# Kernel optimization log

Measured on AMD Instinct MI355X. Metric: run time of the kernel, lower is better.

The kernel has to match this reference:

```python
import jax, jax.numpy as jnp
import numpy as np

N = 8192; E = 131072; K = 20; IN_DIM = 3; HID = 256; N_CLASSES = 32


def setup_inputs():
    key = jax.random.key(0)
    ks = jax.random.split(key, 16)

    def w(k, shape):
        lim = 1.0 / np.sqrt(shape[0])
        return jax.random.uniform(k, shape, jnp.float32, -lim, lim)

    f32 = jnp.float32
    return {
        "features": jax.random.normal(ks[0], (N, IN_DIM), f32),
        "src": jax.random.randint(ks[1], (E,), 0, N, jnp.int32),
        "dst": jax.random.randint(ks[2], (E,), 0, N, jnp.int32),
        # GraphConv params
        "Wc1": w(ks[3], (IN_DIM, HID)), "bc1": jnp.zeros((HID,), f32),
        "Wc2": w(ks[4], (HID, HID)), "bc2": jnp.zeros((HID,), f32),
        "Wc3": w(ks[5], (64, N_CLASSES)), "bc3": jnp.zeros((N_CLASSES,), f32),
        # DynamicEdgeConv 1 MLP: [2*256 -> 256 -> 256], Linear+BN+ReLU each
        "W11": w(ks[6], (2 * HID, 256)), "b11": jnp.zeros((256,), f32), "g11": jnp.ones((256,), f32), "be11": jnp.zeros((256,), f32),
        "W12": w(ks[7], (256, 256)), "b12": jnp.zeros((256,), f32), "g12": jnp.ones((256,), f32), "be12": jnp.zeros((256,), f32),
        # DynamicEdgeConv 2 MLP: [2*256 -> 64 -> 64]
        "W21": w(ks[8], (2 * 256, 64)), "b21": jnp.zeros((64,), f32), "g21": jnp.ones((64,), f32), "be21": jnp.zeros((64,), f32),
        "W22": w(ks[9], (64, 64)), "b22": jnp.zeros((64,), f32), "g22": jnp.ones((64,), f32), "be22": jnp.zeros((64,), f32),
    }


def reference(features, src, dst, Wc1, bc1, Wc2, bc2, Wc3, bc3,
              W11, b11, g11, be11, W12, b12, g12, be12,
              W21, b21, g21, be21, W22, b22, g22, be22):
    n = features.shape[0]
    ones_e = jnp.ones(src.shape[0], features.dtype)
    # DGL GraphConv norm='both': deg clamped to min 1
    dout = jnp.clip(jax.ops.segment_sum(ones_e, src, num_segments=n), 1.0) ** -0.5
    din = jnp.clip(jax.ops.segment_sum(ones_e, dst, num_segments=n), 1.0) ** -0.5

    def gconv(x, W, b, act):
        agg = jax.ops.segment_sum((x * dout[:, None])[src], dst, num_segments=n)
        r = (agg * din[:, None]) @ W + b
        return jax.nn.relu(r) if act else r

    def bn(x, g, b):  # BatchNorm1d in training mode over all edge rows
        mu = jnp.mean(x, axis=(0, 1), keepdims=True)
        var = jnp.mean(jnp.square(x - mu), axis=(0, 1), keepdims=True)
        return (x - mu) * jax.lax.rsqrt(var + 1e-5) * g + b

    def edge_conv(x, layers):
        # dynamic kNN graph on current features (self included, dist 0)
        sq = jnp.sum(x * x, axis=-1)
        d = sq[:, None] + sq[None, :] - 2.0 * (x @ x.T)  # [N,N]
        idx = jax.lax.top_k(-d, K)[1]                    # [N,K]
        xi = x[:, None, :]
        e = jnp.concatenate([jnp.broadcast_to(xi, (n, K, x.shape[-1])), x[idx] - xi], axis=-1)  # [N,K,2F]
        for W, b, g, be in layers:
            e = jax.nn.relu(bn(e @ W + b, g, be))
        return jnp.max(e, axis=1)  # max aggregation over neighbors

    h = gconv(features, Wc1, bc1, True)                                   # [N,256]
    h = edge_conv(h, [(W11, b11, g11, be11), (W12, b12, g12, be12)])      # [N,256]
    h = gconv(h, Wc2, bc2, True)                                          # [N,256]
    h = edge_conv(h, [(W21, b21, g21, be21), (W22, b22, g22, be22)])      # [N,64]
    return gconv(h, Wc3, bc3, False)                                      # [N,32]
```

## Files before the change

### kernel.cpp

```cpp
#include <hip/hip_runtime.h>

#define NN 8192
#define NE 131072
#define KNN 20
#define CH 4096
#define GBM 128
#define GBN 128
#define GBK 64

typedef __attribute__((ext_vector_type(4))) float f32x4;
typedef __attribute__((ext_vector_type(8))) __bf16 bf16x8;

__global__ void k_zero(float* p, int n){
  int i = blockIdx.x*256 + threadIdx.x;
  if (i < n) p[i] = 0.f;
}
__global__ void k_zero_i(int* p, int n){
  int i = blockIdx.x*256 + threadIdx.x;
  if (i < n) p[i] = 0;
}

__device__ __forceinline__ unsigned short f2bf(float x){
  unsigned u = __float_as_uint(x);
  unsigned r = (u + 0x7fff + ((u >> 16) & 1)) >> 16;
  return (unsigned short)r;
}
__device__ __forceinline__ float bf2f(unsigned short h){
  return __uint_as_float((unsigned)h << 16);
}
__device__ __forceinline__ void gload16(const void* g, void* l){
  __builtin_amdgcn_global_load_lds(
      (const __attribute__((address_space(1))) void*)g,
      (__attribute__((address_space(3))) void*)l, 16, 0, 0);
}
__device__ __forceinline__ unsigned mapu(float v){
  unsigned b = __float_as_uint(v);
  return b ^ (((unsigned)((int)b >> 31)) | 0x80000000u);
}
__device__ __forceinline__ float unmapu(unsigned u){
  unsigned b = (u & 0x80000000u) ? (u ^ 0x80000000u) : ~u;
  return __uint_as_float(b);
}

__global__ void k_count(const int* __restrict__ src, const int* __restrict__ dst,
                        int* cs, int* cd){
  int e = blockIdx.x*256 + threadIdx.x;
  if (e < NE){ atomicAdd(&cs[src[e]], 1); atomicAdd(&cd[dst[e]], 1); }
}
__global__ void k_deg(const int* cs, const int* cd, float* dout, float* din){
  int i = blockIdx.x*256 + threadIdx.x;
  if (i < NN){
    dout[i] = rsqrtf((float)max(cs[i], 1));
    din[i]  = rsqrtf((float)max(cd[i], 1));
  }
}
__global__ void k_scan(const int* __restrict__ cnt, int* __restrict__ off){
  __shared__ int sh[256];
  __shared__ int carry;
  int tid = threadIdx.x;
  if (tid == 0) carry = 0;
  __syncthreads();
  for (int base = 0; base < NN; base += 256){
    int v = cnt[base + tid];
    int x = v;
    sh[tid] = x; __syncthreads();
    for (int o = 1; o < 256; o <<= 1){
      int y = (tid >= o) ? sh[tid - o] : 0;
      __syncthreads();
      x += y; sh[tid] = x;
      __syncthreads();
    }
    off[base + tid] = carry + x - v;
    __syncthreads();
    if (tid == 255){
      carry += x;
      if (base + 256 == NN) off[NN] = carry;
    }
    __syncthreads();
  }
}
__global__ void k_fill(const int* __restrict__ src, const int* __restrict__ dst,
                       const int* __restrict__ roff, int* cursor, int* csr){
  int e = blockIdx.x*256 + threadIdx.x;
  if (e < NE){
    int d = dst[e];
    int p = atomicAdd(&cursor[d], 1);
    csr[roff[d] + p] = src[e];
  }
}

__global__ void k_gconv1(const float* __restrict__ feat, const int* __restrict__ roff,
                         const int* __restrict__ csr, const float* __restrict__ dout,
                         const float* __restrict__ din, const float* __restrict__ Wc1,
                         const float* __restrict__ bc1, float* __restrict__ h1){
  int wid = threadIdx.x >> 6, lane = threadIdx.x & 63;
  int i = blockIdx.x*4 + wid;
  float a0=0.f, a1=0.f, a2=0.f;
  int beg = roff[i], end = roff[i+1];
  for (int t = beg + lane; t < end; t += 64){
    int s = csr[t]; float w = dout[s];
    a0 += feat[s*3+0]*w; a1 += feat[s*3+1]*w; a2 += feat[s*3+2]*w;
  }
  for (int m = 32; m; m >>= 1){
    a0 += __shfl_xor(a0, m); a1 += __shfl_xor(a1, m); a2 += __shfl_xor(a2, m);
  }
  float dn = din[i];
  a0 *= dn; a1 *= dn; a2 *= dn;
  for (int c = lane; c < 256; c += 64){
    float r = a0*Wc1[c] + a1*Wc1[256+c] + a2*Wc1[512+c] + bc1[c];
    h1[(size_t)i*256 + c] = fmaxf(r, 0.f);
  }
}

__global__ void k_sq(const float* __restrict__ X, float* __restrict__ sq){
  int wid = threadIdx.x >> 6, lane = threadIdx.x & 63;
  int i = blockIdx.x*4 + wid;
  float4 v = *(const float4*)&X[(size_t)i*256 + lane*4];
  float s = v.x*v.x + v.y*v.y + v.z*v.z + v.w*v.w;
  for (int m = 32; m; m >>= 1) s += __shfl_xor(s, m);
  if (lane == 0) sq[i] = s;
}

__global__ void k_split(const float* __restrict__ X, unsigned short* __restrict__ xcat){
  int row = blockIdx.x, c = threadIdx.x;
  float x = X[(size_t)row*256 + c];
  unsigned short h = f2bf(x);
  unsigned short lo = f2bf(x - bf2f(h));
  xcat[(size_t)row*512 + c] = h;
  xcat[(size_t)row*512 + 256 + c] = lo;
}

__global__ void k_wsplit(const float* __restrict__ W, unsigned short* __restrict__ Whi,
                         unsigned short* __restrict__ Wlo){
  int k = blockIdx.x, n = threadIdx.x;
  float x = W[(size_t)k*256 + n];
  unsigned short h = f2bf(x);
  Whi[(size_t)n*256 + k] = h;
  Wlo[(size_t)n*256 + k] = f2bf(x - bf2f(h));
}
__global__ void k_wsplit64(const float* __restrict__ W, unsigned short* __restrict__ Whi,
                           unsigned short* __restrict__ Wlo){
  int k = blockIdx.x, n = threadIdx.x;
  float x = W[(size_t)k*64 + n];
  unsigned short h = f2bf(x);
  Whi[(size_t)n*64 + k] = h;
  Wlo[(size_t)n*64 + k] = f2bf(x - bf2f(h));
}

__global__ __launch_bounds__(256)
void k_gram_mfma(const unsigned short* __restrict__ Xcat, const float* __restrict__ sq,
                 float* __restrict__ G, int r0){
  __shared__ unsigned short sA[GBM*GBK];
  __shared__ unsigned short sB[GBM*GBK];
  __shared__ float sqr[GBM];
  __shared__ float sqc[GBN];
  int tid = threadIdx.x;
  int lw = tid >> 6, l = tid & 63;
  int rbl = blockIdx.y*GBM;
  int rb = r0 + rbl;
  int cb = blockIdx.x*GBN;

  if (tid < GBM) sqr[tid] = sq[rb + tid];
  else if (tid < GBM + GBN) sqc[tid - GBM] = sq[cb + tid - GBM];

  int srow = l >> 3;
  int scol = (l & 7) ^ srow;
  const unsigned short* srcA[4];
  const unsigned short* srcB[4];
  char* dstA[4]; char* dstB[4];
  #pragma unroll
  for (int i = 0; i < 4; i++){
    int c = lw*4 + i;
    int row = c*8 + srow;
    srcA[i] = Xcat + (size_t)(rb + row)*512 + scol*8;
    srcB[i] = Xcat + (size_t)(cb + row)*512 + scol*8;
    dstA[i] = (char*)sA + c*1024;
    dstB[i] = (char*)sB + c*1024;
  }

  int wm = lw >> 1, wn = lw & 1;
  int fm = l & 15, kg = l >> 4;
  unsigned offA[4][2], offB[4][2];
  #pragma unroll
  for (int mf = 0; mf < 4; mf++){
    int rowa = wm*64 + mf*16 + fm;
    int rowb = wn*64 + mf*16 + fm;
    #pragma unroll
    for (int ks = 0; ks < 2; ks++){
      offA[mf][ks] = rowa*128 + (((unsigned)(ks*4 + kg) ^ (rowa & 7)))*16;
      offB[mf][ks] = rowb*128 + (((unsigned)(ks*4 + kg) ^ (rowb & 7)))*16;
    }
  }

  f32x4 acc[4][4];
  #pragma unroll
  for (int m = 0; m < 4; m++)
    #pragma unroll
    for (int n = 0; n < 4; n++) acc[m][n] = (f32x4){0.f,0.f,0.f,0.f};

  #pragma unroll
  for (int s = 0; s < 12; s++){
    int sec = s >> 2;
    int inner = (s & 3)*64;
    int cbA = (sec == 1 ? 256 : 0) + inner;
    int cbB = (sec == 2 ? 256 : 0) + inner;
    #pragma unroll
    for (int i = 0; i < 4; i++){
      gload16(srcA[i] + cbA, dstA[i]);
      gload16(srcB[i] + cbB, dstB[i]);
    }
    __syncthreads();
    #pragma unroll
    for (int ks = 0; ks < 2; ks++){
      bf16x8 a[4], b[4];
      #pragma unroll
      for (int mf = 0; mf < 4; mf++) a[mf] = *(const bf16x8*)((const char*)sA + offA[mf][ks]);
      #pragma unroll
      for (int nf = 0; nf < 4; nf++) b[nf] = *(const bf16x8*)((const char*)sB + offB[nf][ks]);
      #pragma unroll
      for (int mf = 0; mf < 4; mf++)
        #pragma unroll
        for (int nf = 0; nf < 4; nf++)
          acc[mf][nf] = __builtin_amdgcn_mfma_f32_16x16x32_bf16(a[mf], b[nf], acc[mf][nf], 0, 0, 0);
    }
    __syncthreads();
  }

  #pragma unroll
  for (int mf = 0; mf < 4; mf++){
    int lr0 = wm*64 + mf*16 + kg*4;
    #pragma unroll
    for (int nf = 0; nf < 4; nf++){
      int lc = wn*64 + nf*16 + fm;
      float sc = sqc[lc];
      #pragma unroll
      for (int r = 0; r < 4; r++)
        G[(size_t)(rbl + lr0 + r)*NN + cb + lc] = (sqr[lr0 + r] + sc) - 2.f*acc[mf][nf][r];
    }
  }
}

__global__ __launch_bounds__(256)
void k_topk(const float* __restrict__ G, int r0, int* __restrict__ idxo){
  int tid = threadIdx.x;
  int wid = tid >> 6, lane = tid & 63;
  int rl = blockIdx.x*4 + wid;
  int gr = r0 + rl;
  const float4* row4 = (const float4*)(G + (size_t)rl*NN);

  float kd0=INFINITY,kd1=INFINITY,kd2=INFINITY,kd3=INFINITY,kd4=INFINITY,
        kd5=INFINITY,kd6=INFINITY,kd7=INFINITY,kd8=INFINITY,kd9=INFINITY,
        kd10=INFINITY,kd11=INFINITY,kd12=INFINITY,kd13=INFINITY,kd14=INFINITY,
        kd15=INFINITY,kd16=INFINITY,kd17=INFINITY,kd18=INFINITY,kd19=INFINITY;
  int ki0=0x7fffffff,ki1=0x7fffffff,ki2=0x7fffffff,ki3=0x7fffffff,ki4=0x7fffffff,
      ki5=0x7fffffff,ki6=0x7fffffff,ki7=0x7fffffff,ki8=0x7fffffff,ki9=0x7fffffff,
      ki10=0x7fffffff,ki11=0x7fffffff,ki12=0x7fffffff,ki13=0x7fffffff,ki14=0x7fffffff,
      ki15=0x7fffffff,ki16=0x7fffffff,ki17=0x7fffffff,ki18=0x7fffffff,ki19=0x7fffffff;

#define ST(U) { bool sw = nk < kd##U; float tv = kd##U; int tq = ki##U; \
      if (sw){ kd##U = nk; ki##U = ni; nk = tv; ni = tq; } }
#define INSE(kc, jc) { if ((kc) < kd19){ float nk = (kc); int ni = (jc); \
      ST(0) ST(1) ST(2) ST(3) ST(4) ST(5) ST(6) ST(7) ST(8) ST(9) \
      ST(10) ST(11) ST(12) ST(13) ST(14) ST(15) ST(16) ST(17) ST(18) ST(19) } }

  float4 g0c = row4[lane];
  float4 g1c = row4[lane + 64];
  #pragma unroll 1
  for (int o = 0; o < 16; o++){
    float4 g0 = g0c, g1 = g1c;
    if (o < 15){
      g0c = row4[lane + (o+1)*128];
      g1c = row4[lane + 64 + (o+1)*128];
    }
    int jb0 = (lane + o*128)*4;
    int jb1 = (lane + 64 + o*128)*4;
    float t19 = kd19;
    float mn = fminf(fminf(fminf(g0.x, g0.y), fminf(g0.z, g0.w)),
                     fminf(fminf(g1.x, g1.y), fminf(g1.z, g1.w)));
    if (__any(mn < t19)){
      INSE(g0.x, jb0+0);
      INSE(g0.y, jb0+1);
      INSE(g0.z, jb0+2);
      INSE(g0.w, jb0+3);
      INSE(g1.x, jb1+0);
      INSE(g1.y, jb1+1);
      INSE(g1.z, jb1+2);
      INSE(g1.w, jb1+3);
    }
  }
#undef INSE
#undef ST

#define MV(A,B) { kd##A = kd##B; ki##A = ki##B; }
  #pragma unroll 1
  for (int r = 0; r < KNN; r++){
    float bv = kd0; int bi = ki0;
    #pragma unroll
    for (int mm = 32; mm; mm >>= 1){
      float ov = __shfl_xor(bv, mm); int oi = __shfl_xor(bi, mm);
      if (ov < bv || (ov == bv && oi < bi)){ bv = ov; bi = oi; }
    }
    if (ki0 == bi){
      MV(0,1) MV(1,2) MV(2,3) MV(3,4) MV(4,5) MV(5,6) MV(6,7) MV(7,8) MV(8,9) MV(9,10)
      MV(10,11) MV(11,12) MV(12,13) MV(13,14) MV(14,15) MV(15,16) MV(16,17) MV(17,18) MV(18,19)
      kd19 = INFINITY; ki19 = 0x7fffffff;
    }
    if (lane == 0) idxo[(size_t)gr*KNN + r] = bi;
  }
#undef MV
}

__global__ void k_wd(const float* __restrict__ W, float* __restrict__ Wd, int rows, int M){
  int t = blockIdx.x*256 + threadIdx.x;
  if (t < rows*M) Wd[t] = W[t] - W[rows*M + t];
}

__global__ __launch_bounds__(256)
void k_mm_mfma(const unsigned short* __restrict__ Xc, const unsigned short* __restrict__ Wthi,
               const unsigned short* __restrict__ Wtlo, const float* __restrict__ bias,
               float* __restrict__ C, int relu){
  int tid = threadIdx.x;
  int lw = tid >> 6, l = tid & 63;
  int wm = lw >> 1, wn = lw & 1;
  int fm = l & 15, kg = l >> 4;
  int rb = blockIdx.x*32;

  const unsigned short* aptr = Xc + (size_t)(rb + wm*16 + fm)*512 + kg*8;
  const unsigned short* bhi[8];
  const unsigned short* blo[8];
  float bz[8];
  #pragma unroll
  for (int nf = 0; nf < 8; nf++){
    int col = wn*128 + nf*16 + fm;
    bhi[nf] = Wthi + (size_t)col*256 + kg*8;
    blo[nf] = Wtlo + (size_t)col*256 + kg*8;
    bz[nf] = bias ? bias[col] : 0.f;
  }

  f32x4 acc[8];
  #pragma unroll
  for (int n = 0; n < 8; n++) acc[n] = (f32x4){0.f,0.f,0.f,0.f};

  #pragma unroll 1
  for (int sec = 0; sec < 3; sec++){
    int ka = (sec == 1) ? 256 : 0;
    int bsec = (sec == 2);
    #pragma unroll
    for (int st = 0; st < 8; st++){
      bf16x8 a = *(const bf16x8*)(aptr + ka + st*32);
      #pragma unroll
      for (int nf = 0; nf < 8; nf++){
        const unsigned short* bp = bsec ? blo[nf] : bhi[nf];
        bf16x8 b = *(const bf16x8*)(bp + st*32);
        acc[nf] = __builtin_amdgcn_mfma_f32_16x16x32_bf16(a, b, acc[nf], 0, 0, 0);
      }
    }
  }

  #pragma unroll
  for (int nf = 0; nf < 8; nf++){
    int col = wn*128 + nf*16 + fm;
    #pragma unroll
    for (int r = 0; r < 4; r++){
      int row = rb + wm*16 + kg*4 + r;
      float v = acc[nf][r] + bz[nf];
      if (relu) v = fmaxf(v, 0.f);
      C[(size_t)row*256 + col] = v;
    }
  }
}

__global__ __launch_bounds__(256)
void k_mm(const float* __restrict__ A, const float* __restrict__ B,
          const float* __restrict__ bias, float* __restrict__ Cout,
          int n, int Kd, int M, int relu){
  __shared__ float la[16][68], lb[16][68];
  int tid = threadIdx.x;
  int rb = blockIdx.y*64, cb = blockIdx.x*64;
  int lr = tid >> 2, lq = (tid & 3)*4;
  int ty = tid >> 4, tx = tid & 15;
  float acc[4][4] = {};
  for (int k0 = 0; k0 < Kd; k0 += 16){
    __syncthreads();
    #pragma unroll
    for (int u = 0; u < 4; u++){
      int k = k0 + lq + u;
      la[lq+u][lr] = (k < Kd) ? A[(size_t)(rb+lr)*Kd + k] : 0.f;
    }
    int kk = tid >> 4; int cc = (tid & 15)*4;
    #pragma unroll
    for (int u = 0; u < 4; u++){
      int c = cb + cc + u; int k = k0 + kk;
      lb[kk][cc+u] = (k < Kd && c < M) ? B[(size_t)k*M + c] : 0.f;
    }
    __syncthreads();
    #pragma unroll
    for (int k = 0; k < 16; k++){
      float4 a = *(const float4*)&la[k][ty*4];
      float4 b = *(const float4*)&lb[k][tx*4];
      float avv[4] = {a.x,a.y,a.z,a.w}, bvv[4] = {b.x,b.y,b.z,b.w};
      #pragma unroll
      for (int u = 0; u < 4; u++)
        #pragma unroll
        for (int v = 0; v < 4; v++) acc[u][v] += avv[u]*bvv[v];
    }
  }
  #pragma unroll
  for (int u = 0; u < 4; u++){
    int r = rb + ty*4 + u;
    #pragma unroll
    for (int v = 0; v < 4; v++){
      int c = cb + tx*4 + v;
      if (c < M){
        float x = acc[u][v] + (bias ? bias[c] : 0.f);
        if (relu) x = fmaxf(x, 0.f);
        Cout[(size_t)r*M + c] = x;
      }
    }
  }
}

template<int C>
__global__ __launch_bounds__(256)
void k_stats1(const float* __restrict__ A, const float* __restrict__ P,
              const int* __restrict__ idx, float* __restrict__ ssum, float* __restrict__ ssq){
  __shared__ int si[128], sj[128];
  int tid = threadIdx.x;
  int s0 = blockIdx.x*128;
  if (tid < 128){ si[tid] = (s0 + tid)/KNN; sj[tid] = idx[s0 + tid]; }
  __syncthreads();
  constexpr int MPAR = 256/C;
  int tc = tid % C, sr = tid / C;
  float s = 0.f, q = 0.f;
  for (int m = sr; m < 128; m += MPAR){
    float v = A[(size_t)si[m]*C + tc] + P[(size_t)sj[m]*C + tc];
    s += v; q += v*v;
  }
  if constexpr (MPAR > 1){
    __shared__ float rs[256], rq[256];
    rs[tid] = s; rq[tid] = q; __syncthreads();
    if (sr == 0){
      for (int u = 1; u < MPAR; u++){ s += rs[u*C + tc]; q += rq[u*C + tc]; }
    }
  }
  if (sr == 0){ atomicAdd(&ssum[tc], s); atomicAdd(&ssq[tc], q); }
}

__global__ void k_bn_final(const float* __restrict__ ssum, const float* __restrict__ ssq,
                           const float* __restrict__ g, const float* __restrict__ be,
                           float* __restrict__ sb, float* __restrict__ tb, int C, float invn){
  int c = threadIdx.x;
  if (c < C){
    float mu = ssum[c]*invn;
    float var = fmaxf(ssq[c]*invn - mu*mu, 0.f);
    float s = g[c]*rsqrtf(var + 1e-5f);
    sb[c] = s; tb[c] = be[c] - mu*s;
  }
}

__global__ __launch_bounds__(256, 2)
void k_edge_mfma(const float* __restrict__ A, const float* __restrict__ P,
                 const int* __restrict__ idx, const float* __restrict__ sb,
                 const float* __restrict__ tb, const unsigned short* __restrict__ Wthi,
                 const unsigned short* __restrict__ Wtlo, const float* __restrict__ bias,
                 unsigned* __restrict__ h2u, float* __restrict__ ssum, float* __restrict__ ssq){
  __shared__ unsigned short ehi[64*256];
  __shared__ unsigned short elo[64*256];
  __shared__ int sj[64];
  int tid = threadIdx.x;
  int lw = tid >> 6, l = tid & 63;
  int s0 = blockIdx.x*64;
  if (tid < 64) sj[tid] = idx[s0 + tid];
  float sbc = sb[tid], tbc = tb[tid];
  __syncthreads();

  #pragma unroll 1
  for (int g = 0; g < 8; g++){
    float va[8];
    #pragma unroll
    for (int u = 0; u < 8; u++){
      int it = g*8 + u;
      int i = (s0 + it)/KNN;
      int j = sj[it];
      va[u] = A[(size_t)i*256 + tid] + P[(size_t)j*256 + tid];
    }
    #pragma unroll
    for (int u = 0; u < 8; u++){
      int it = g*8 + u;
      float v = fmaxf(va[u]*sbc + tbc, 0.f);
      unsigned short h = f2bf(v);
      unsigned short lo = f2bf(v - bf2f(h));
      unsigned off = (unsigned)it*512 + (((unsigned)tid*2) ^ (((unsigned)it & 7) << 4));
      *(unsigned short*)((char*)ehi + off) = h;
      *(unsigned short*)((char*)elo + off) = lo;
    }
  }
  __syncthreads();

  int fm = l & 15, kg = l >> 4;
  const unsigned short* bhi[4];
  const unsigned short* blo[4];
  float bz[4];
  #pragma unroll
  for (int nf = 0; nf < 4; nf++){
    int col = lw*64 + nf*16 + fm;
    bhi[nf] = Wthi + (size_t)col*256 + kg*8;
    blo[nf] = Wtlo + (size_t)col*256 + kg*8;
    bz[nf] = bias[col];
  }

  f32x4 acc[4][4];
  #pragma unroll
  for (int m = 0; m < 4; m++)
    #pragma unroll
    for (int n = 0; n < 4; n++) acc[m][n] = (f32x4){0.f,0.f,0.f,0.f};

  #pragma unroll 1
  for (int sec = 0; sec < 3; sec++){
    const char* abase = (sec == 1) ? (const char*)elo : (const char*)ehi;
    int bsec = (sec == 2);
    #pragma unroll 1
    for (int st = 0; st < 8; st++){
      int g = st*4 + kg;
      bf16x8 a[4], b[4];
      #pragma unroll
      for (int mf = 0; mf < 4; mf++){
        int row = mf*16 + fm;
        a[mf] = *(const bf16x8*)(abase + row*512 + ((unsigned)(g ^ (row & 7)))*16);
      }
      #pragma unroll
      for (int nf = 0; nf < 4; nf++){
        const unsigned short* bp = bsec ? blo[nf] : bhi[nf];
        b[nf] = *(const bf16x8*)(bp + st*32);
      }
      #pragma unroll
      for (int mf = 0; mf < 4; mf++)
        #pragma unroll
        for (int nf = 0; nf < 4; nf++)
          acc[mf][nf] = __builtin_amdgcn_mfma_f32_16x16x32_bf16(a[mf], b[nf], acc[mf][nf], 0, 0, 0);
    }
  }

  float s4[4], q4[4];
  #pragma unroll
  for (int nf = 0; nf < 4; nf++){ s4[nf] = 0.f; q4[nf] = 0.f; }
  #pragma unroll
  for (int mf = 0; mf < 4; mf++){
    int gR = s0 + mf*16 + kg*4;
    int n0 = gR/20, n3 = (gR+3)/20;
    int kk = n3*20 - gR;
    #pragma unroll
    for (int nf = 0; nf < 4; nf++){
      int col = lw*64 + nf*16 + fm;
      float v0 = acc[mf][nf][0] + bz[nf];
      float v1 = acc[mf][nf][1] + bz[nf];
      float v2 = acc[mf][nf][2] + bz[nf];
      float v3 = acc[mf][nf][3] + bz[nf];
      s4[nf] += v0 + v1 + v2 + v3;
      q4[nf] += v0*v0 + v1*v1 + v2*v2 + v3*v3;
      if (n0 == n3){
        float m = fmaxf(fmaxf(v0, v1), fmaxf(v2, v3));
        atomicMax(&h2u[(size_t)n0*256 + col], mapu(m));
      } else {
        float lo = v0, hi = v3;
        if (1 < kk) lo = fmaxf(lo, v1); else hi = fmaxf(hi, v1);
        if (2 < kk) lo = fmaxf(lo, v2); else hi = fmaxf(hi, v2);
        atomicMax(&h2u[(size_t)n0*256 + col], mapu(lo));
        atomicMax(&h2u[(size_t)n3*256 + col], mapu(hi));
      }
    }
  }
  #pragma unroll
  for (int nf = 0; nf < 4; nf++){
    s4[nf] += __shfl_xor(s4[nf], 16); q4[nf] += __shfl_xor(q4[nf], 16);
    s4[nf] += __shfl_xor(s4[nf], 32); q4[nf] += __shfl_xor(q4[nf], 32);
  }
  if (kg == 0){
    #pragma unroll
    for (int nf = 0; nf < 4; nf++){
      int col = lw*64 + nf*16 + fm;
      atomicAdd(&ssum[col], s4[nf]);
      atomicAdd(&ssq[col], q4[nf]);
    }
  }
}

__global__ void k_h2final(const unsigned* __restrict__ h2u, const float* __restrict__ sb,
                          const float* __restrict__ tb, float* __restrict__ h2){
  int n = blockIdx.x, c = threadIdx.x;
  float x = unmapu(h2u[(size_t)n*256 + c]);
  h2[(size_t)n*256 + c] = fmaxf(sb[c]*x + tb[c], 0.f);
}

__global__ __launch_bounds__(256, 2)
void k_edge_mfma64(const float* __restrict__ A, const float* __restrict__ P,
                   const int* __restrict__ idx, const float* __restrict__ sb,
                   const float* __restrict__ tb, const unsigned short* __restrict__ Wthi,
                   const unsigned short* __restrict__ Wtlo, const float* __restrict__ bias,
                   unsigned* __restrict__ h4u, float* __restrict__ ssum, float* __restrict__ ssq){
  __shared__ unsigned short ehi[128*64];
  __shared__ unsigned short elo[128*64];
  __shared__ int sj[128];
  int tid = threadIdx.x;
  int lw = tid >> 6, l = tid & 63;
  int s0 = blockIdx.x*128;
  if (tid < 128) sj[tid] = idx[s0 + tid];
  int col0 = tid & 63, rgrp = tid >> 6;
  float sbc = sb[col0], tbc = tb[col0];
  __syncthreads();

  #pragma unroll 1
  for (int g = 0; g < 4; g++){
    float va[8];
    #pragma unroll
    for (int u = 0; u < 8; u++){
      int it = (g*8 + u)*4 + rgrp;
      int i = (s0 + it)/KNN;
      int j = sj[it];
      va[u] = A[(size_t)i*64 + col0] + P[(size_t)j*64 + col0];
    }
    #pragma unroll
    for (int u = 0; u < 8; u++){
      int it = (g*8 + u)*4 + rgrp;
      float v = fmaxf(va[u]*sbc + tbc, 0.f);
      unsigned short h = f2bf(v);
      unsigned short lo = f2bf(v - bf2f(h));
      unsigned off = (unsigned)it*128 + (((unsigned)col0*2) ^ (((unsigned)it & 7) << 4));
      *(unsigned short*)((char*)ehi + off) = h;
      *(unsigned short*)((char*)elo + off) = lo;
    }
  }
  __syncthreads();

  int wm = lw >> 1, wn = lw & 1;
  int fm = l & 15, kg = l >> 4;
  const unsigned short* bhi[2];
  const unsigned short* blo[2];
  float bz[2];
  #pragma unroll
  for (int nf = 0; nf < 2; nf++){
    int col = wn*32 + nf*16 + fm;
    bhi[nf] = Wthi + (size_t)col*64 + kg*8;
    blo[nf] = Wtlo + (size_t)col*64 + kg*8;
    bz[nf] = bias[col];
  }

  f32x4 acc[4][2];
  #pragma unroll
  for (int m = 0; m < 4; m++)
    #pragma unroll
    for (int n = 0; n < 2; n++) acc[m][n] = (f32x4){0.f,0.f,0.f,0.f};

  #pragma unroll 1
  for (int sec = 0; sec < 3; sec++){
    const char* abase = (sec == 1) ? (const char*)elo : (const char*)ehi;
    int bsec = (sec == 2);
    #pragma unroll
    for (int ks = 0; ks < 2; ks++){
      int g = ks*4 + kg;
      bf16x8 a[4], b[2];
      #pragma unroll
      for (int mf = 0; mf < 4; mf++){
        int row = wm*64 + mf*16 + fm;
        a[mf] = *(const bf16x8*)(abase + row*128 + ((unsigned)(g ^ (row & 7)))*16);
      }
      #pragma unroll
      for (int nf = 0; nf < 2; nf++){
        const unsigned short* bp = bsec ? blo[nf] : bhi[nf];
        b[nf] = *(const bf16x8*)(bp + ks*32);
      }
      #pragma unroll
      for (int mf = 0; mf < 4; mf++)
        #pragma unroll
        for (int nf = 0; nf < 2; nf++)
          acc[mf][nf] = __builtin_amdgcn_mfma_f32_16x16x32_bf16(a[mf], b[nf], acc[mf][nf], 0, 0, 0);
    }
  }

  float s2[2], q2[2];
  #pragma unroll
  for (int nf = 0; nf < 2; nf++){ s2[nf] = 0.f; q2[nf] = 0.f; }
  #pragma unroll
  for (int mf = 0; mf < 4; mf++){
    int gR = s0 + wm*64 + mf*16 + kg*4;
    int n0 = gR/20, n3 = (gR+3)/20;
    int kk = n3*20 - gR;
    #pragma unroll
    for (int nf = 0; nf < 2; nf++){
      int col = wn*32 + nf*16 + fm;
      float v0 = acc[mf][nf][0] + bz[nf];
      float v1 = acc[mf][nf][1] + bz[nf];
      float v2 = acc[mf][nf][2] + bz[nf];
      float v3 = acc[mf][nf][3] + bz[nf];
      s2[nf] += v0 + v1 + v2 + v3;
      q2[nf] += v0*v0 + v1*v1 + v2*v2 + v3*v3;
      if (n0 == n3){
        float m = fmaxf(fmaxf(v0, v1), fmaxf(v2, v3));
        atomicMax(&h4u[(size_t)n0*64 + col], mapu(m));
      } else {
        float lo = v0, hi = v3;
        if (1 < kk) lo = fmaxf(lo, v1); else hi = fmaxf(hi, v1);
        if (2 < kk) lo = fmaxf(lo, v2); else hi = fmaxf(hi, v2);
        atomicMax(&h4u[(size_t)n0*64 + col], mapu(lo));
        atomicMax(&h4u[(size_t)n3*64 + col], mapu(hi));
      }
    }
  }
  #pragma unroll
  for (int nf = 0; nf < 2; nf++){
    s2[nf] += __shfl_xor(s2[nf], 16); q2[nf] += __shfl_xor(q2[nf], 16);
    s2[nf] += __shfl_xor(s2[nf], 32); q2[nf] += __shfl_xor(q2[nf], 32);
  }
  if (kg == 0){
    #pragma unroll
    for (int nf = 0; nf < 2; nf++){
      int col = wn*32 + nf*16 + fm;
      atomicAdd(&ssum[col], s2[nf]);
      atomicAdd(&ssq[col], q2[nf]);
    }
  }
}

__global__ void k_h4final(const unsigned* __restrict__ h4u, const float* __restrict__ sb,
                          const float* __restrict__ tb, float* __restrict__ h4){
  int n = blockIdx.x*4 + (threadIdx.x >> 6), c = threadIdx.x & 63;
  float x = unmapu(h4u[(size_t)n*64 + c]);
  h4[(size_t)n*64 + c] = fmaxf(sb[c]*x + tb[c], 0.f);
}

template<int C>
__global__ void k_agg(const float* __restrict__ X, const int* __restrict__ roff,
                      const int* __restrict__ csr, const float* __restrict__ dout,
                      const float* __restrict__ din, float* __restrict__ XA){
  int i = blockIdx.x; int c = threadIdx.x;
  float acc = 0.f;
  int b = roff[i], e = roff[i+1];
  for (int t = b; t < e; t++){
    int s = csr[t];
    acc += X[(size_t)s*C + c]*dout[s];
  }
  XA[(size_t)i*C + c] = acc*din[i];
}

extern "C" void kernel_launch(void* const* d_in, const int* in_sizes, int n_in,
                              void* d_out, int out_size, void* d_ws, size_t ws_size,
                              hipStream_t stream){
  const float* feat = (const float*)d_in[0];
  const int*   src  = (const int*)d_in[1];
  const int*   dst  = (const int*)d_in[2];
  const float* Wc1  = (const float*)d_in[3];
  const float* bc1  = (const float*)d_in[4];
  const float* Wc2  = (const float*)d_in[5];
  const float* bc2  = (const float*)d_in[6];
  const float* Wc3  = (const float*)d_in[7];
  const float* bc3  = (const float*)d_in[8];
  const float* W11  = (const float*)d_in[9];
  const float* b11  = (const float*)d_in[10];
  const float* g11  = (const float*)d_in[11];
  const float* be11 = (const float*)d_in[12];
  const float* W12  = (const float*)d_in[13];
  const float* b12  = (const float*)d_in[14];
  const float* g12  = (const float*)d_in[15];
  const float* be12 = (const float*)d_in[16];
  const float* W21  = (const float*)d_in[17];
  const float* b21  = (const float*)d_in[18];
  const float* g21  = (const float*)d_in[19];
  const float* be21 = (const float*)d_in[20];
  const float* W22  = (const float*)d_in[21];
  const float* b22  = (const float*)d_in[22];
  const float* g22  = (const float*)d_in[23];
  const float* be22 = (const float*)d_in[24];
  float* out = (float*)d_out;

  char* w = (char*)d_ws; size_t off = 0;
  auto alloc = [&](size_t bytes)->void*{
    void* p = w + off;
    off += bytes; off = (off + 255) & ~(size_t)255;
    return p;
  };
  int* cnt_s  = (int*)alloc(NN*4);
  int* cnt_d  = (int*)alloc(NN*4);
  int* roff   = (int*)alloc((NN+1)*4);
  int* cursor = (int*)alloc(NN*4);
  int* csr    = (int*)alloc(NE*4);
  int* idx    = (int*)alloc((size_t)NN*KNN*4);
  float* dout = (float*)alloc(NN*4);
  float* din  = (float*)alloc(NN*4);
  float* sqv  = (float*)alloc(NN*4);
  float* h1   = (float*)alloc((size_t)NN*256*4);
  float* h2   = (float*)alloc((size_t)NN*256*4);
  float* h3   = (float*)alloc((size_t)NN*256*4);
  float* h4   = (float*)alloc((size_t)NN*64*4);
  float* xa   = (float*)alloc((size_t)NN*256*4);
  float* Abuf = (float*)alloc((size_t)NN*256*4);
  float* Pbuf = (float*)alloc((size_t)NN*256*4);
  float* Wd   = (float*)alloc(256*256*4);
  float* ssum = (float*)alloc(256*4);
  float* ssq  = (float*)alloc(256*4);
  float* sbn  = (float*)alloc(256*4);
  float* tbn  = (float*)alloc(256*4);
  unsigned* h2u = (unsigned*)alloc((size_t)NN*256*4);
  unsigned* h4u = (unsigned*)alloc((size_t)NN*64*4);
  unsigned short* wthi = (unsigned short*)alloc(256*256*2);
  unsigned short* wtlo = (unsigned short*)alloc(256*256*2);
  unsigned short* wdhi = (unsigned short*)alloc(256*256*2);
  unsigned short* wdlo = (unsigned short*)alloc(256*256*2);
  unsigned short* wbhi = (unsigned short*)alloc(256*256*2);
  unsigned short* wblo = (unsigned short*)alloc(256*256*2);
  unsigned short* wchi = (unsigned short*)alloc(256*256*2);
  unsigned short* wclo = (unsigned short*)alloc(256*256*2);
  unsigned short* w64hi = (unsigned short*)alloc(64*64*2);
  unsigned short* w64lo = (unsigned short*)alloc(64*64*2);
  float* scratch = (float*)alloc((size_t)NN*KNN*256*4);
  float* gram = scratch;
  unsigned short* xcat = (unsigned short*)(scratch + (size_t)CH*NN);
  (void)ws_size; (void)n_in; (void)in_sizes; (void)out_size;

  const float invn = 1.0f / (float)(NN*KNN);

  k_zero_i<<<32, 256, 0, stream>>>(cnt_s, NN);
  k_zero_i<<<32, 256, 0, stream>>>(cnt_d, NN);
  k_zero_i<<<32, 256, 0, stream>>>(cursor, NN);
  k_count<<<NE/256, 256, 0, stream>>>(src, dst, cnt_s, cnt_d);
  k_deg<<<32, 256, 0, stream>>>(cnt_s, cnt_d, dout, din);
  k_scan<<<1, 256, 0, stream>>>(cnt_d, roff);
  k_fill<<<NE/256, 256, 0, stream>>>(src, dst, roff, cursor, csr);

  k_gconv1<<<NN/4, 256, 0, stream>>>(feat, roff, csr, dout, din, Wc1, bc1, h1);

  k_sq<<<NN/4, 256, 0, stream>>>(h1, sqv);
  k_split<<<NN, 256, 0, stream>>>(h1, xcat);
  for (int r0 = 0; r0 < NN; r0 += CH){
    k_gram_mfma<<<dim3(NN/GBN, CH/GBM), 256, 0, stream>>>(xcat, sqv, gram, r0);
    k_topk<<<CH/4, 256, 0, stream>>>(gram, r0, idx);
  }
  k_wd<<<256, 256, 0, stream>>>(W11, Wd, 256, 256);
  k_wsplit<<<256, 256, 0, stream>>>(Wd, wdhi, wdlo);
  k_wsplit<<<256, 256, 0, stream>>>(W11 + 256*256, wbhi, wblo);
  k_wsplit<<<256, 256, 0, stream>>>(W12, wthi, wtlo);
  k_mm_mfma<<<NN/32, 256, 0, stream>>>(xcat, wdhi, wdlo, b11, Abuf, 0);
  k_mm_mfma<<<NN/32, 256, 0, stream>>>(xcat, wbhi, wblo, nullptr, Pbuf, 0);
  k_zero<<<2, 256, 0, stream>>>(ssum, 256); k_zero<<<2, 256, 0, stream>>>(ssq, 256);
  k_stats1<256><<<NN*KNN/128, 256, 0, stream>>>(Abuf, Pbuf, idx, ssum, ssq);
  k_bn_final<<<1, 256, 0, stream>>>(ssum, ssq, g11, be11, sbn, tbn, 256, invn);
  k_zero<<<2, 256, 0, stream>>>(ssum, 256); k_zero<<<2, 256, 0, stream>>>(ssq, 256);
  k_zero_i<<<NN, 256, 0, stream>>>((int*)h2u, NN*256);
  k_edge_mfma<<<NN*KNN/64, 256, 0, stream>>>(Abuf, Pbuf, idx, sbn, tbn, wthi, wtlo, b12, h2u, ssum, ssq);
  k_bn_final<<<1, 256, 0, stream>>>(ssum, ssq, g12, be12, sbn, tbn, 256, invn);
  k_h2final<<<NN, 256, 0, stream>>>(h2u, sbn, tbn, h2);

  k_agg<256><<<NN, 256, 0, stream>>>(h2, roff, csr, dout, din, xa);
  k_split<<<NN, 256, 0, stream>>>(xa, xcat);
  k_wsplit<<<256, 256, 0, stream>>>(Wc2, wchi, wclo);
  k_mm_mfma<<<NN/32, 256, 0, stream>>>(xcat, wchi, wclo, bc2, h3, 1);

  k_sq<<<NN/4, 256, 0, stream>>>(h3, sqv);
  k_split<<<NN, 256, 0, stream>>>(h3, xcat);
  for (int r0 = 0; r0 < NN; r0 += CH){
    k_gram_mfma<<<dim3(NN/GBN, CH/GBM), 256, 0, stream>>>(xcat, sqv, gram, r0);
    k_topk<<<CH/4, 256, 0, stream>>>(gram, r0, idx);
  }
  k_wd<<<64, 256, 0, stream>>>(W21, Wd, 256, 64);
  k_wsplit64<<<64, 64, 0, stream>>>(W22, w64hi, w64lo);
  k_mm<<<dim3(1, NN/64), 256, 0, stream>>>(h3, Wd, b21, Abuf, NN, 256, 64, 0);
  k_mm<<<dim3(1, NN/64), 256, 0, stream>>>(h3, W21 + 256*64, nullptr, Pbuf, NN, 256, 64, 0);
  k_zero<<<2, 256, 0, stream>>>(ssum, 256); k_zero<<<2, 256, 0, stream>>>(ssq, 256);
  k_stats1<64><<<NN*KNN/128, 256, 0, stream>>>(Abuf, Pbuf, idx, ssum, ssq);
  k_bn_final<<<1, 256, 0, stream>>>(ssum, ssq, g21, be21, sbn, tbn, 64, invn);
  k_zero<<<2, 256, 0, stream>>>(ssum, 256); k_zero<<<2, 256, 0, stream>>>(ssq, 256);
  k_zero_i<<<NN/4, 256, 0, stream>>>((int*)h4u, NN*64);
  k_edge_mfma64<<<NN*KNN/128, 256, 0, stream>>>(Abuf, Pbuf, idx, sbn, tbn, w64hi, w64lo, b22, h4u, ssum, ssq);
  k_bn_final<<<1, 256, 0, stream>>>(ssum, ssq, g22, be22, sbn, tbn, 64, invn);
  k_h4final<<<NN/4, 256, 0, stream>>>(h4u, sbn, tbn, h4);

  k_agg<64><<<NN, 64, 0, stream>>>(h4, roff, csr, dout, din, xa);
  k_mm<<<dim3(1, NN/64), 256, 0, stream>>>(xa, Wc3, bc3, out, NN, 64, 32, 0);
}
```

Baseline: 1.430 ms.

## Fuse Gram tile computation with per-tile partial top-k and add merge kernel

Instead of writing the full NxN distance matrix in row chunks and then scanning each row for the 20 nearest, each Gram tile block now writes its distances into shared memory and extracts a partial top-20 per row over its 128 columns. A new merge kernel combines the 64 partial lists per row into the final kNN indices. This removes the large distance-matrix write and reread, but adds a serial insertion sort per tile, extra syncs and shared-memory reuse, plus a partial-result buffer that is itself sizeable.

```diff
diff --git a/kernel.cpp b/kernel.cpp
--- a/kernel.cpp
+++ b/kernel.cpp
@@ -3,7 +3,6 @@
 #define NN 8192
 #define NE 131072
 #define KNN 20
-#define CH 4096
 #define GBM 128
 #define GBN 128
 #define GBK 64
@@ -148,16 +147,16 @@
 }
 
 __global__ __launch_bounds__(256)
-void k_gram_mfma(const unsigned short* __restrict__ Xcat, const float* __restrict__ sq,
-                 float* __restrict__ G, int r0){
-  __shared__ unsigned short sA[GBM*GBK];
-  __shared__ unsigned short sB[GBM*GBK];
+void k_gramtopk(const unsigned short* __restrict__ Xcat, const float* __restrict__ sq,
+                float* __restrict__ pd, int* __restrict__ pi){
+  __shared__ __align__(16) float keytile[64][132];
   __shared__ float sqr[GBM];
   __shared__ float sqc[GBN];
+  unsigned short* sA = (unsigned short*)&keytile[0][0];
+  unsigned short* sB = sA + GBM*GBK;
   int tid = threadIdx.x;
   int lw = tid >> 6, l = tid & 63;
-  int rbl = blockIdx.y*GBM;
-  int rb = r0 + rbl;
+  int rb = blockIdx.y*GBM;
   int cb = blockIdx.x*GBN;
 
   if (tid < GBM) sqr[tid] = sq[rb + tid];
@@ -226,70 +225,88 @@
     __syncthreads();
   }
 
-  #pragma unroll
-  for (int mf = 0; mf < 4; mf++){
-    int lr0 = wm*64 + mf*16 + kg*4;
-    #pragma unroll
-    for (int nf = 0; nf < 4; nf++){
-      int lc = wn*64 + nf*16 + fm;
-      float sc = sqc[lc];
-      #pragma unroll
-      for (int r = 0; r < 4; r++)
-        G[(size_t)(rbl + lr0 + r)*NN + cb + lc] = (sqr[lr0 + r] + sc) - 2.f*acc[mf][nf][r];
-    }
-  }
-}
-
-__global__ __launch_bounds__(256)
-void k_topk(const float* __restrict__ G, int r0, int* __restrict__ idxo){
-  int tid = threadIdx.x;
-  int wid = tid >> 6, lane = tid & 63;
-  int rl = blockIdx.x*4 + wid;
-  int gr = r0 + rl;
-  const float4* row4 = (const float4*)(G + (size_t)rl*NN);
-
-  float kd0=INFINITY,kd1=INFINITY,kd2=INFINITY,kd3=INFINITY,kd4=INFINITY,
-        kd5=INFINITY,kd6=INFINITY,kd7=INFINITY,kd8=INFINITY,kd9=INFINITY,
-        kd10=INFINITY,kd11=INFINITY,kd12=INFINITY,kd13=INFINITY,kd14=INFINITY,
-        kd15=INFINITY,kd16=INFINITY,kd17=INFINITY,kd18=INFINITY,kd19=INFINITY;
-  int ki0=0x7fffffff,ki1=0x7fffffff,ki2=0x7fffffff,ki3=0x7fffffff,ki4=0x7fffffff,
-      ki5=0x7fffffff,ki6=0x7fffffff,ki7=0x7fffffff,ki8=0x7fffffff,ki9=0x7fffffff,
-      ki10=0x7fffffff,ki11=0x7fffffff,ki12=0x7fffffff,ki13=0x7fffffff,ki14=0x7fffffff,
-      ki15=0x7fffffff,ki16=0x7fffffff,ki17=0x7fffffff,ki18=0x7fffffff,ki19=0x7fffffff;
-
 #define ST(U) { bool sw = nk < kd##U; float tv = kd##U; int tq = ki##U; \
       if (sw){ kd##U = nk; ki##U = ni; nk = tv; ni = tq; } }
 #define INSE(kc, jc) { if ((kc) < kd19){ float nk = (kc); int ni = (jc); \
       ST(0) ST(1) ST(2) ST(3) ST(4) ST(5) ST(6) ST(7) ST(8) ST(9) \
       ST(10) ST(11) ST(12) ST(13) ST(14) ST(15) ST(16) ST(17) ST(18) ST(19) } }
-
-  float4 g0c = row4[lane];
-  float4 g1c = row4[lane + 64];
+#define MV(A,B) { kd##A = kd##B; ki##A = ki##B; }
   #pragma unroll 1
-  for (int o = 0; o < 16; o++){
-    float4 g0 = g0c, g1 = g1c;
-    if (o < 15){
-      g0c = row4[lane + (o+1)*128];
-      g1c = row4[lane + 64 + (o+1)*128];
-    }
-    int jb0 = (lane + o*128)*4;
-    int jb1 = (lane + 64 + o*128)*4;
-    float t19 = kd19;
-    float mn = fminf(fminf(fminf(g0.x, g0.y), fminf(g0.z, g0.w)),
-                     fminf(fminf(g1.x, g1.y), fminf(g1.z, g1.w)));
-    if (__any(mn < t19)){
-      INSE(g0.x, jb0+0);
-      INSE(g0.y, jb0+1);
-      INSE(g0.z, jb0+2);
-      INSE(g0.w, jb0+3);
-      INSE(g1.x, jb1+0);
-      INSE(g1.y, jb1+1);
-      INSE(g1.z, jb1+2);
-      INSE(g1.w, jb1+3);
-    }
-  }
+  for (int p = 0; p < 2; p++){
+    if (wm == p){
+      #pragma unroll
+      for (int mf = 0; mf < 4; mf++){
+        int lr0 = mf*16 + kg*4;
+        #pragma unroll
+        for (int nf = 0; nf < 4; nf++){
+          int lc = wn*64 + nf*16 + fm;
+          float sc = sqc[lc];
+          #pragma unroll
+          for (int r = 0; r < 4; r++)
+            keytile[lr0 + r][lc] = (sqr[p*64 + lr0 + r] + sc) - 2.f*acc[mf][nf][r];
+        }
+      }
+    }
+    __syncthreads();
+    if (wm == p){
+      int rowl = wn*32 + (l >> 1);
+      int half = l & 1;
+      const float* krow = &keytile[rowl][half*64];
+      int jb0 = cb + half*64;
+      float kd0=INFINITY,kd1=INFINITY,kd2=INFINITY,kd3=INFINITY,kd4=INFINITY,
+            kd5=INFINITY,kd6=INFINITY,kd7=INFINITY,kd8=INFINITY,kd9=INFINITY,
+            kd10=INFINITY,kd11=INFINITY,kd12=INFINITY,kd13=INFINITY,kd14=INFINITY,
+            kd15=INFINITY,kd16=INFINITY,kd17=INFINITY,kd18=INFINITY,kd19=INFINITY;
+      int ki0=0x7fffffff,ki1=0x7fffffff,ki2=0x7fffffff,ki3=0x7fffffff,ki4=0x7fffffff,
+          ki5=0x7fffffff,ki6=0x7fffffff,ki7=0x7fffffff,ki8=0x7fffffff,ki9=0x7fffffff,
+          ki10=0x7fffffff,ki11=0x7fffffff,ki12=0x7fffffff,ki13=0x7fffffff,ki14=0x7fffffff,
+          ki15=0x7fffffff,ki16=0x7fffffff,ki17=0x7fffffff,ki18=0x7fffffff,ki19=0x7fffffff;
+      #pragma unroll 1
+      for (int st = 0; st < 16; st++){
+        float4 kv = *(const float4*)&krow[st*4];
+        int jb = jb0 + st*4;
+        INSE(kv.x, jb+0);
+        INSE(kv.y, jb+1);
+        INSE(kv.z, jb+2);
+        INSE(kv.w, jb+3);
+      }
+      size_t pbase = ((size_t)(rb + p*64 + rowl)*64 + blockIdx.x)*20;
+      #pragma unroll 1
+      for (int r = 0; r < KNN; r++){
+        float bv = kd0; int bi = ki0;
+        float ov = __shfl_xor(bv, 1); int oi = __shfl_xor(bi, 1);
+        if (ov < bv || (ov == bv && oi < bi)){ bv = ov; bi = oi; }
+        if (ki0 == bi){
+          MV(0,1) MV(1,2) MV(2,3) MV(3,4) MV(4,5) MV(5,6) MV(6,7) MV(7,8) MV(8,9) MV(9,10)
+          MV(10,11) MV(11,12) MV(12,13) MV(13,14) MV(14,15) MV(15,16) MV(16,17) MV(17,18) MV(18,19)
+          kd19 = INFINITY; ki19 = 0x7fffffff;
+        }
+        if (half == 0){ pd[pbase + r] = bv; pi[pbase + r] = bi; }
+      }
+    }
+    __syncthreads();
+  }
+#undef MV
 #undef INSE
 #undef ST
+}
+
+__global__ __launch_bounds__(256)
+void k_knn_merge(const float* __restrict__ pd, const int* __restrict__ pi,
+                 int* __restrict__ idxo){
+  int tid = threadIdx.x, wid = tid >> 6, l = tid & 63;
+  int row = blockIdx.x*4 + wid;
+  size_t base = ((size_t)row*64 + l)*20;
+  const float4* pdv = (const float4*)&pd[base];
+  const int4*   piv = (const int4*)&pi[base];
+  float4 a0 = pdv[0], a1 = pdv[1], a2 = pdv[2], a3 = pdv[3], a4 = pdv[4];
+  int4   b0 = piv[0], b1 = piv[1], b2 = piv[2], b3 = piv[3], b4 = piv[4];
+  float kd0=a0.x,kd1=a0.y,kd2=a0.z,kd3=a0.w,kd4=a1.x,kd5=a1.y,kd6=a1.z,kd7=a1.w,
+        kd8=a2.x,kd9=a2.y,kd10=a2.z,kd11=a2.w,kd12=a3.x,kd13=a3.y,kd14=a3.z,kd15=a3.w,
+        kd16=a4.x,kd17=a4.y,kd18=a4.z,kd19=a4.w;
+  int ki0=b0.x,ki1=b0.y,ki2=b0.z,ki3=b0.w,ki4=b1.x,ki5=b1.y,ki6=b1.z,ki7=b1.w,
+      ki8=b2.x,ki9=b2.y,ki10=b2.z,ki11=b2.w,ki12=b3.x,ki13=b3.y,ki14=b3.z,ki15=b3.w,
+      ki16=b4.x,ki17=b4.y,ki18=b4.z,ki19=b4.w;
 
 #define MV(A,B) { kd##A = kd##B; ki##A = ki##B; }
   #pragma unroll 1
@@ -305,7 +322,7 @@
       MV(10,11) MV(11,12) MV(12,13) MV(13,14) MV(14,15) MV(15,16) MV(16,17) MV(17,18) MV(18,19)
       kd19 = INFINITY; ki19 = 0x7fffffff;
     }
-    if (lane == 0) idxo[(size_t)gr*KNN + r] = bi;
+    if (l == 0) idxo[(size_t)row*KNN + r] = bi;
   }
 #undef MV
 }
@@ -811,9 +828,9 @@
   unsigned short* wclo = (unsigned short*)alloc(256*256*2);
   unsigned short* w64hi = (unsigned short*)alloc(64*64*2);
   unsigned short* w64lo = (unsigned short*)alloc(64*64*2);
-  float* scratch = (float*)alloc((size_t)NN*KNN*256*4);
-  float* gram = scratch;
-  unsigned short* xcat = (unsigned short*)(scratch + (size_t)CH*NN);
+  float* pd = (float*)alloc((size_t)NN*64*KNN*4);
+  int*   pi = (int*)alloc((size_t)NN*64*KNN*4);
+  unsigned short* xcat = (unsigned short*)alloc((size_t)NN*512*2);
   (void)ws_size; (void)n_in; (void)in_sizes; (void)out_size;
 
   const float invn = 1.0f / (float)(NN*KNN);
@@ -830,10 +847,8 @@
 
   k_sq<<<NN/4, 256, 0, stream>>>(h1, sqv);
   k_split<<<NN, 256, 0, stream>>>(h1, xcat);
-  for (int r0 = 0; r0 < NN; r0 += CH){
-    k_gram_mfma<<<dim3(NN/GBN, CH/GBM), 256, 0, stream>>>(xcat, sqv, gram, r0);
-    k_topk<<<CH/4, 256, 0, stream>>>(gram, r0, idx);
-  }
+  k_gramtopk<<<dim3(NN/GBN, NN/GBM), 256, 0, stream>>>(xcat, sqv, pd, pi);
+  k_knn_merge<<<NN/4, 256, 0, stream>>>(pd, pi, idx);
   k_wd<<<256, 256, 0, stream>>>(W11, Wd, 256, 256);
   k_wsplit<<<256, 256, 0, stream>>>(Wd, wdhi, wdlo);
   k_wsplit<<<256, 256, 0, stream>>>(W11 + 256*256, wbhi, wblo);
@@ -856,10 +871,8 @@
 
   k_sq<<<NN/4, 256, 0, stream>>>(h3, sqv);
   k_split<<<NN, 256, 0, stream>>>(h3, xcat);
-  for (int r0 = 0; r0 < NN; r0 += CH){
-    k_gram_mfma<<<dim3(NN/GBN, CH/GBM), 256, 0, stream>>>(xcat, sqv, gram, r0);
-    k_topk<<<CH/4, 256, 0, stream>>>(gram, r0, idx);
-  }
+  k_gramtopk<<<dim3(NN/GBN, NN/GBM), 256, 0, stream>>>(xcat, sqv, pd, pi);
+  k_knn_merge<<<NN/4, 256, 0, stream>>>(pd, pi, idx);
   k_wd<<<64, 256, 0, stream>>>(W21, Wd, 256, 64);
   k_wsplit64<<<64, 64, 0, stream>>>(W22, w64hi, w64lo);
   k_mm<<<dim3(1, NN/64), 256, 0, stream>>>(h3, Wd, b21, Abuf, NN, 256, 64, 0);
```

After: 2.078 ms. 45.4% more time.
